# Kernel optimization log

Hardware: AMD Instinct MI355X
Metric: run time of the kernel (lower is better)

## Reference

```python
import jax, jax.numpy as jnp
import numpy as np

NEG = -1e30  # stand-in for -inf that keeps gradients finite


def setup_inputs() -> dict:
    key = jax.random.key(0)
    k0, k1, k2 = jax.random.split(key, 3)
    B, S, W, K = 48, 128, 4, 256
    logits = jax.random.normal(k0, (B, S, W, K), dtype=jnp.float32)
    T = jax.random.normal(k1, (B, K, K), dtype=jnp.float32)
    hamming_cost = jax.random.uniform(k2, (B, S, W, K), dtype=jnp.float32)
    tag_mask = jnp.ones((B, K, K), dtype=jnp.float32)
    text_mask = jnp.ones((B, S), dtype=jnp.int32)
    return dict(logits=logits, T=T, hamming_cost=hamming_cost,
                tag_mask=tag_mask, text_mask=text_mask)


def reference(logits, T, hamming_cost, tag_mask, text_mask):
    # Semi-Markov CRF partition function (use_transition_layer == 'True').
    B, S, W, K = logits.shape
    lg = jnp.transpose(logits, (1, 2, 0, 3))        # (S, W, B, K)
    hc = jnp.transpose(hamming_cost, (1, 2, 0, 3))  # (S, W, B, K)
    # emission score for a span of width w+1 ending at j, labeled k
    emit_all = (lg + hc) * tag_mask[:, 0, :]        # (S, W, B, K)
    tranT = T * tag_mask                            # (B, K, Kprev)
    w_idx = jnp.arange(W)

    # buf[w] = alpha[j - w]; rows with j - w < 0 held at NEG (excluded)
    buf0 = jnp.full((W, B, K), NEG, dtype=jnp.float32).at[0].set(0.0)

    def step(buf, inp):
        emit_j, j = inp  # emit_j: (W, B, K)
        # transition applies only when the previous alpha is a real segment
        # boundary (w < j); the w == j row connects to the initial state.
        tran = jnp.where((w_idx < j)[:, None, None, None], tranT[None], 0.0)
        # scores[w, b, k, kp] = alpha[j-w, b, kp] + T'[b, k, kp] + emit[w, b, k]
        scores = buf[:, :, None, :] + tran + emit_j[:, :, :, None]
        alpha_j = jax.nn.logsumexp(scores, axis=(0, 3))  # (B, K)
        buf = jnp.concatenate([alpha_j[None], buf[:-1]], axis=0)
        return buf, alpha_j

    _, alphas = jax.lax.scan(step, buf0, (emit_all, jnp.arange(S)))
    full = jnp.concatenate([jnp.zeros((1, B, K), dtype=jnp.float32), alphas], axis=0)
    ls = jax.nn.logsumexp(full, axis=-1)            # (S+1, B)
    lengths = jnp.sum(text_mask, axis=1)            # (B,)
    partition = ls[lengths, jnp.arange(B)]          # (B,)
    return partition[None]                          # (1, B) as in torch code
```

## Files before the change

kernel.cpp:

```cpp
#include <hip/hip_runtime.h>
#include <hip/hip_bf16.h>
#include <type_traits>

typedef __attribute__((ext_vector_type(8))) _Float16 half8;
typedef __attribute__((ext_vector_type(4))) _Float16 half4;
typedef __attribute__((ext_vector_type(2))) _Float16 half2;
typedef __attribute__((ext_vector_type(4))) float f32x4;

constexpr int CB = 48, CS = 128, CW = 4, CK = 256;
constexpr int LDP = 264;

__global__ void prep_eT_kernel(const f32x4* __restrict__ T,
                               const f32x4* __restrict__ tm,
                               half4* __restrict__ eT, int n4) {
    int i = blockIdx.x * 256 + threadIdx.x;
    if (i < n4) {
        f32x4 t = T[i], m = tm[i];
        half4 o;
        o[0] = (_Float16)__expf(t[0] * m[0]);
        o[1] = (_Float16)__expf(t[1] * m[1]);
        o[2] = (_Float16)__expf(t[2] * m[2]);
        o[3] = (_Float16)__expf(t[3] * m[3]);
        eT[i] = o;
    }
}

__global__ __launch_bounds__(256, 1)
void crf_scan_kernel(const float* __restrict__ logits,
                     const float* __restrict__ ham,
                     const _Float16* __restrict__ eT,
                     const float* __restrict__ tag_mask,
                     const int* __restrict__ text_mask,
                     float* __restrict__ out) {
    const int b = blockIdx.x;
    const int tid = (int)threadIdx.x;
    const int wv = tid >> 6;
    const int lane = tid & 63;
    const int l16 = lane & 15;
    const int g4 = lane >> 4;

    __shared__ alignas(16) _Float16 ebuf[16 * LDP];
    __shared__ alignas(16) float ylds[CK][4];
    __shared__ float red[4];
    __shared__ int len_s;

    for (int i = tid; i < 16 * LDP; i += 256) ebuf[i] = (_Float16)0.0f;
    if (tid == 0) len_s = 0;
    __syncthreads();
    ebuf[3 * LDP + tid] = (_Float16)1.0f;
    if (tid < CS) atomicAdd(&len_s, text_mask[b * CS + tid]);

    const float tm0 = tag_mask[(size_t)b * CK * CK + tid];

    half8 bfr[8][4];
    const _Float16* eTb = eT + (size_t)b * CK * CK;
#pragma unroll
    for (int c = 0; c < 8; ++c)
#pragma unroll
        for (int t = 0; t < 4; ++t) {
            int k = wv * 64 + t * 16 + l16;
            bfr[c][t] = *(const half8*)(eTb + (size_t)k * CK + c * 32 + g4 * 8);
        }

    const float* lgb = logits + (size_t)b * CS * CW * CK;
    const float* hcb = ham    + (size_t)b * CS * CW * CK;

    float mr[4] = {0.0f, 0.0f, 0.0f, 0.0f};
    float ls_prev = __logf(256.0f) - 2.0f;
    float out_r = __logf(256.0f);
    float e_last = 0.0f, M_last = 0.0f;

    float em_cur[4];
#pragma unroll
    for (int w = 0; w < 4; ++w)
        em_cur[w] = (lgb[w * CK + tid] + hcb[w * CK + tid]) * tm0;

    __syncthreads();
    const int len = len_s;

    const half2 one2 = {(_Float16)1.0f, (_Float16)1.0f};

    auto step = [&](int j, auto uc, auto firstc) {
        constexpr int u = uc.value;
        constexpr bool first = firstc.value;
        constexpr int sp = (u + 3) & 3;

        half8 af[8];
#pragma unroll
        for (int c = 0; c < 8; ++c)
            af[c] = *(const half8*)(ebuf + l16 * LDP + c * 32 + g4 * 8);

        int jn = (j + 1 < CS) ? j + 1 : 0;
        float lgn[4], hcn[4];
#pragma unroll
        for (int w = 0; w < 4; ++w) {
            int idx = jn * (CW * CK) + w * CK + tid;
            lgn[w] = lgb[idx];
            hcn[w] = hcb[idx];
        }

        float rs0 = 0.0f, rs1 = 0.0f;
#pragma unroll
        for (int c = 0; c < 8; ++c) {
#pragma unroll
            for (int p = 0; p < 4; p += 2) {
                half2 h0 = {af[c][2 * p], af[c][2 * p + 1]};
                half2 h1 = {af[c][2 * p + 2], af[c][2 * p + 3]};
                rs0 = __builtin_amdgcn_fdot2(h0, one2, rs0, false);
                rs1 = __builtin_amdgcn_fdot2(h1, one2, rs1, false);
            }
        }
        float rs = rs0 + rs1;
        rs += __shfl_xor(rs, 16, 64);
        rs += __shfl_xor(rs, 32, 64);
        float sum_prev = __shfl(rs, sp, 64);

        float lsj = mr[sp] + __logf(sum_prev);
        if (j == len) out_r = lsj;
        float delta = lsj - ls_prev;
        ls_prev = lsj;
        float Mj = lsj + delta;
        float C = mr[sp];

        f32x4 acc[4];
#pragma unroll
        for (int t = 0; t < 4; ++t) acc[t] = (f32x4){0.0f, 0.0f, 0.0f, 0.0f};
#pragma unroll
        for (int c = 0; c < 8; ++c)
#pragma unroll
            for (int t = 0; t < 4; ++t)
                acc[t] = __builtin_amdgcn_mfma_f32_16x16x32_f16(af[c], bfr[c][t], acc[t], 0, 0, 0);

        if (lane < 16) {
#pragma unroll
            for (int t = 0; t < 4; ++t)
                *(f32x4*)(&ylds[wv * 64 + t * 16 + l16][0]) = acc[t];
        }
        f32x4 y = *(const f32x4*)(&ylds[tid][0]);

        float S = 0.0f;
#pragma unroll
        for (int w = 0; w < 4; ++w) {
            const int sw = (u + 3 - w) & 3;
            float yv = y[sw];
            if (first) {
                if (w == j) yv = 256.0f;
                else if (w > j) yv = 0.0f;
            }
            S = fmaf(yv, __expf(mr[sw] + em_cur[w] - C), S);
        }
        float e = S * __expf(C - Mj);
        ebuf[u * LDP + tid] = (_Float16)e;
        e_last = e;
        M_last = Mj;
        mr[u] = Mj;

#pragma unroll
        for (int w = 0; w < 4; ++w)
            em_cur[w] = (lgn[w] + hcn[w]) * tm0;

        __syncthreads();
    };

#define IC(v) std::integral_constant<int, v>{}
#define BC(v) std::integral_constant<bool, v>{}
    step(0, IC(0), BC(true));
    step(1, IC(1), BC(true));
    step(2, IC(2), BC(true));
    step(3, IC(3), BC(true));
    for (int jj = 4; jj < CS; jj += 4) {
        step(jj + 0, IC(0), BC(false));
        step(jj + 1, IC(1), BC(false));
        step(jj + 2, IC(2), BC(false));
        step(jj + 3, IC(3), BC(false));
    }
#undef IC
#undef BC

    float s = e_last;
#pragma unroll
    for (int o = 32; o; o >>= 1) s += __shfl_xor(s, o, 64);
    if (lane == 0) red[wv] = s;
    __syncthreads();
    if (tid == 0) {
        float tot = red[0] + red[1] + red[2] + red[3];
        float ls_full = M_last + __logf(tot);
        if (len == CS) out_r = ls_full;
        out[b] = out_r;
    }
}

extern "C" void kernel_launch(void* const* d_in, const int* in_sizes, int n_in,
                              void* d_out, int out_size, void* d_ws, size_t ws_size,
                              hipStream_t stream) {
    const float* logits    = (const float*)d_in[0];
    const float* T         = (const float*)d_in[1];
    const float* ham       = (const float*)d_in[2];
    const float* tag_mask  = (const float*)d_in[3];
    const int*   text_mask = (const int*)d_in[4];
    float* out = (float*)d_out;

    _Float16* eT = (_Float16*)d_ws;
    int n4 = CB * CK * CK / 4;
    prep_eT_kernel<<<(n4 + 255) / 256, 256, 0, stream>>>(
        (const f32x4*)T, (const f32x4*)tag_mask, (half4*)eT, n4);
    crf_scan_kernel<<<CB, 256, 0, stream>>>(logits, ham, eT, tag_mask, text_mask, out);
}
```

Baseline: 197.8 us.

## Keep MFMA A-fragments in registers, read outputs directly, prefetch emissions four steps ahead

Instead of reloading the full 16-row A operand from LDS each step, each lane keeps its half8 fragments in registers and only the lanes whose row matches the newly needed alpha row reload from LDS. The MFMA accumulators are read directly per lane via lane-group selection, which removes the LDS round-trip through ylds. Emission loads are prefetched four steps ahead in a register ring, and the exponentials of the emission terms are hoisted ahead of the MFMA. The block barrier becomes a raw s_barrier with an explicit lgkmcnt wait, which lowers per-step latency on the serial chain but relies on the accumulator lane mapping and manual synchronisation being correct.

```diff
diff --git a/kernel.cpp b/kernel.cpp
--- a/kernel.cpp
+++ b/kernel.cpp
@@ -39,16 +39,14 @@
     const int l16 = lane & 15;
     const int g4 = lane >> 4;
 
-    __shared__ alignas(16) _Float16 ebuf[16 * LDP];
-    __shared__ alignas(16) float ylds[CK][4];
+    __shared__ alignas(16) _Float16 ebuf[4 * LDP];
     __shared__ float red[4];
     __shared__ int len_s;
 
-    for (int i = tid; i < 16 * LDP; i += 256) ebuf[i] = (_Float16)0.0f;
     if (tid == 0) len_s = 0;
     __syncthreads();
+    if (tid < CS) atomicAdd(&len_s, text_mask[b * CS + tid]);
     ebuf[3 * LDP + tid] = (_Float16)1.0f;
-    if (tid < CS) atomicAdd(&len_s, text_mask[b * CS + tid]);
 
     const float tm0 = tag_mask[(size_t)b * CK * CK + tid];
 
@@ -64,16 +62,31 @@
 
     const float* lgb = logits + (size_t)b * CS * CW * CK;
     const float* hcb = ham    + (size_t)b * CS * CW * CK;
+
+    half8 af[8];
+    {
+        const _Float16 iv = ((l16 & 3) == 3) ? (_Float16)1.0f : (_Float16)0.0f;
+        half8 v;
+#pragma unroll
+        for (int i = 0; i < 8; ++i) v[i] = iv;
+#pragma unroll
+        for (int c = 0; c < 8; ++c) af[c] = v;
+    }
 
     float mr[4] = {0.0f, 0.0f, 0.0f, 0.0f};
     float ls_prev = __logf(256.0f) - 2.0f;
     float out_r = __logf(256.0f);
     float e_last = 0.0f, M_last = 0.0f;
 
-    float em_cur[4];
-#pragma unroll
-    for (int w = 0; w < 4; ++w)
-        em_cur[w] = (lgb[w * CK + tid] + hcb[w * CK + tid]) * tm0;
+    float lgp[4][4], hcp[4][4];
+#pragma unroll
+    for (int s = 0; s < 4; ++s)
+#pragma unroll
+        for (int w = 0; w < 4; ++w) {
+            int idx = s * (CW * CK) + w * CK + tid;
+            lgp[s][w] = lgb[idx];
+            hcp[s][w] = hcb[idx];
+        }
 
     __syncthreads();
     const int len = len_s;
@@ -85,19 +98,32 @@
         constexpr bool first = firstc.value;
         constexpr int sp = (u + 3) & 3;
 
-        half8 af[8];
-#pragma unroll
-        for (int c = 0; c < 8; ++c)
-            af[c] = *(const half8*)(ebuf + l16 * LDP + c * 32 + g4 * 8);
-
-        int jn = (j + 1 < CS) ? j + 1 : 0;
-        float lgn[4], hcn[4];
-#pragma unroll
-        for (int w = 0; w < 4; ++w) {
-            int idx = jn * (CW * CK) + w * CK + tid;
-            lgn[w] = lgb[idx];
-            hcn[w] = hcb[idx];
-        }
+        if ((l16 & 3) == sp) {
+#pragma unroll
+            for (int c = 0; c < 8; ++c)
+                af[c] = *(const half8*)(ebuf + sp * LDP + c * 32 + g4 * 8);
+        }
+
+        float em_w[4];
+#pragma unroll
+        for (int w = 0; w < 4; ++w)
+            em_w[w] = (lgp[u][w] + hcp[u][w]) * tm0;
+
+        {
+            int jn = (j + 4 < CS) ? j + 4 : 0;
+#pragma unroll
+            for (int w = 0; w < 4; ++w) {
+                int idx = jn * (CW * CK) + w * CK + tid;
+                lgp[u][w] = lgb[idx];
+                hcp[u][w] = hcb[idx];
+            }
+        }
+
+        const float C = mr[sp];
+        float E[4];
+#pragma unroll
+        for (int r = 0; r < 4; ++r)
+            E[r] = __expf(mr[r] + em_w[(u + 3 - r) & 3] - C);
 
         float rs0 = 0.0f, rs1 = 0.0f;
 #pragma unroll
@@ -115,12 +141,12 @@
         rs += __shfl_xor(rs, 32, 64);
         float sum_prev = __shfl(rs, sp, 64);
 
-        float lsj = mr[sp] + __logf(sum_prev);
+        float lsj = C + __logf(sum_prev);
         if (j == len) out_r = lsj;
         float delta = lsj - ls_prev;
         ls_prev = lsj;
         float Mj = lsj + delta;
-        float C = mr[sp];
+        float scl = __expf(C - Mj);
 
         f32x4 acc[4];
 #pragma unroll
@@ -131,35 +157,28 @@
             for (int t = 0; t < 4; ++t)
                 acc[t] = __builtin_amdgcn_mfma_f32_16x16x32_f16(af[c], bfr[c][t], acc[t], 0, 0, 0);
 
-        if (lane < 16) {
-#pragma unroll
-            for (int t = 0; t < 4; ++t)
-                *(f32x4*)(&ylds[wv * 64 + t * 16 + l16][0]) = acc[t];
-        }
-        f32x4 y = *(const f32x4*)(&ylds[tid][0]);
-
         float S = 0.0f;
 #pragma unroll
-        for (int w = 0; w < 4; ++w) {
-            const int sw = (u + 3 - w) & 3;
-            float yv = y[sw];
+        for (int r = 0; r < 4; ++r) {
+            float v01 = (g4 & 1) ? acc[1][r] : acc[0][r];
+            float v23 = (g4 & 1) ? acc[3][r] : acc[2][r];
+            float yv  = (g4 & 2) ? v23 : v01;
             if (first) {
+                const int w = (u + 3 - r) & 3;
                 if (w == j) yv = 256.0f;
                 else if (w > j) yv = 0.0f;
             }
-            S = fmaf(yv, __expf(mr[sw] + em_cur[w] - C), S);
-        }
-        float e = S * __expf(C - Mj);
+            S = fmaf(yv, E[r], S);
+        }
+        float e = S * scl;
         ebuf[u * LDP + tid] = (_Float16)e;
         e_last = e;
         M_last = Mj;
         mr[u] = Mj;
 
-#pragma unroll
-        for (int w = 0; w < 4; ++w)
-            em_cur[w] = (lgn[w] + hcn[w]) * tm0;
-
-        __syncthreads();
+        asm volatile("s_waitcnt lgkmcnt(0)" ::: "memory");
+        __builtin_amdgcn_s_barrier();
+        __builtin_amdgcn_sched_barrier(0);
     };
 
 #define IC(v) std::integral_constant<int, v>{}
```

Result: faster. 193.5 us (-2.2%).
